# Kernel tuning notes

Measured on AMD Instinct MI355X. Metric: run time of the kernel, lower is better.

Reference implementation:

```python
import jax, jax.numpy as jnp
import numpy as np

B, C, H, W = 8, 256, 64, 64
GROUPS = 32
EPS = 1e-6


def setup_inputs() -> dict:
    key = jax.random.key(0)
    ks = jax.random.split(key, 8)
    s = 0.02
    return {
        "x": jax.random.normal(ks[0], (B, C, H, W), dtype=jnp.float32),
        "gn_scale": jnp.ones((C,), jnp.float32),
        "gn_bias": jnp.zeros((C,), jnp.float32),
        "wq": jax.random.normal(ks[1], (C, C), jnp.float32) * s,
        "bq": jnp.zeros((C,), jnp.float32),
        "wk": jax.random.normal(ks[2], (C, C), jnp.float32) * s,
        "bk": jnp.zeros((C,), jnp.float32),
        "wv": jax.random.normal(ks[3], (C, C), jnp.float32) * s,
        "bv": jnp.zeros((C,), jnp.float32),
        "wproj": jax.random.normal(ks[4], (C, C), jnp.float32) * s,
        "bproj": jnp.zeros((C,), jnp.float32),
    }


def _group_norm(x, scale, bias):
    b, c, h, w = x.shape
    xg = x.reshape(b, GROUPS, c // GROUPS, h, w)
    mean = xg.mean(axis=(2, 3, 4), keepdims=True)
    var = xg.var(axis=(2, 3, 4), keepdims=True)
    xn = ((xg - mean) * jax.lax.rsqrt(var + EPS)).reshape(b, c, h, w)
    return xn * scale[None, :, None, None] + bias[None, :, None, None]


def _conv1x1(x, w, b):
    # 1x1 conv == channel-mixing matmul: w is [out_ch, in_ch]
    return jnp.einsum("oc,bchw->bohw", w, x) + b[None, :, None, None]


def reference(x, gn_scale, gn_bias, wq, bq, wk, bk, wv, bv, wproj, bproj):
    b, c, h, w = x.shape
    hn = _group_norm(x, gn_scale, gn_bias)
    q = _conv1x1(hn, wq, bq).reshape(b, c, h * w)  # [b,c,n]
    k = _conv1x1(hn, wk, bk).reshape(b, c, h * w)
    v = _conv1x1(hn, wv, bv).reshape(b, c, h * w)
    # scores[b,n,m] = <q[:, :, n], k[:, :, m]> * c^-0.5  (softmax over keys m)
    scale = jnp.asarray(c, x.dtype) ** -0.5
    attn = jax.nn.softmax(jnp.einsum("bcn,bcm->bnm", q, k) * scale, axis=2)
    # h_[b,c,n] = sum_m v[b,c,m] * attn[b,n,m]
    h_ = jnp.einsum("bcm,bnm->bcn", v, attn).reshape(b, c, h, w)
    h_ = _conv1x1(h_, wproj, bproj)
    return x + h_
```

## Files before the change

### kernel.cpp

```cpp
#include <hip/hip_runtime.h>

#define B_ 8
#define C_ 256
#define N_ 4096
#define G_ 32

typedef __bf16 bf16;
typedef __bf16 bf16x8 __attribute__((ext_vector_type(8)));
typedef float f32x4 __attribute__((ext_vector_type(4)));
typedef long i64;
typedef long i64x2 __attribute__((ext_vector_type(2)));
typedef unsigned int u32;
typedef unsigned char u8;
typedef unsigned short u16;
typedef unsigned long long u64;
typedef long __attribute__((may_alias)) i64a;

__device__ __forceinline__ f32x4 mfma16(bf16x8 a, bf16x8 b, f32x4 c) {
    return __builtin_amdgcn_mfma_f32_16x16x32_bf16(a, b, c, 0, 0, 0);
}
__device__ __forceinline__ f32x4 mfma_fp8(i64 a, i64 b, f32x4 c) {
    return __builtin_amdgcn_mfma_f32_16x16x32_fp8_fp8(a, b, c, 0, 0, 0);
}

typedef __attribute__((address_space(1))) const void* gas_t;
typedef __attribute__((address_space(3))) void* las_t;
__device__ __forceinline__ void gl2lds16(const void* g, void* l) {
    __builtin_amdgcn_global_load_lds((gas_t)g, (las_t)l, 16, 0, 0);
}

__device__ __forceinline__ u32 f32_to_fp8(float x) {
    union { float f; u32 u; } c;
    c.f = x;
    u32 s = (c.u >> 24) & 0x80;
    u32 m = (c.u & 0x7fffffff) + 0x00080000;
    int e = (int)(m >> 23) - 127;
    if (e < -6) return s;
    if (e > 8) return s | 0x7e;
    u32 v = ((u32)(e + 7) << 3) | ((m >> 20) & 7);
    if (v > 0x7e) v = 0x7e;
    return s | v;
}
__device__ __forceinline__ u32 fp8_fast(float x) {
    union { float f; u32 u; } c;
    c.f = x;
    return ((c.u + 0x00080000u) >> 20) - 960u;
}

__global__ __launch_bounds__(256) void gn_stats(const float* __restrict__ x,
                                                float* __restrict__ gstats) {
    int blk = blockIdx.x;
    int b = blk >> 5, g = blk & 31;
    int tid = threadIdx.x;
    int c = g * 8 + (tid >> 5);
    const float* row = x + ((size_t)(b * C_ + c)) * N_;
    float s = 0.f, s2 = 0.f;
    for (int n = (tid & 31) * 4; n < N_; n += 128) {
        float4 v = *(const float4*)(row + n);
        s += v.x + v.y + v.z + v.w;
        s2 += v.x * v.x + v.y * v.y + v.z * v.z + v.w * v.w;
    }
    for (int off = 32; off; off >>= 1) {
        s += __shfl_xor(s, off);
        s2 += __shfl_xor(s2, off);
    }
    __shared__ float red[8];
    int wid = tid >> 6;
    if ((tid & 63) == 0) { red[wid] = s; red[4 + wid] = s2; }
    __syncthreads();
    if (tid == 0) {
        float S = red[0] + red[1] + red[2] + red[3];
        float S2 = red[4] + red[5] + red[6] + red[7];
        float mean = S * (1.f / 32768.f);
        float var = S2 * (1.f / 32768.f) - mean * mean;
        gstats[blk * 2] = mean;
        gstats[blk * 2 + 1] = rsqrtf(var + 1e-6f);
    }
}

__global__ __launch_bounds__(256) void gn_apply(const float* __restrict__ x,
                                                const float* __restrict__ gsc,
                                                const float* __restrict__ gbi,
                                                const float* __restrict__ gstats,
                                                bf16* __restrict__ hn) {
    __shared__ float tile[32][33];
    int b = blockIdx.z, c0 = blockIdx.y * 32, n0 = blockIdx.x * 32;
    int tx = threadIdx.x & 31, ty = threadIdx.x >> 5;
    for (int i = 0; i < 4; i++) {
        int cl = ty + i * 8;
        int c = c0 + cl;
        int g = c >> 3;
        float mean = gstats[(b * G_ + g) * 2];
        float rstd = gstats[(b * G_ + g) * 2 + 1];
        float sc = gsc[c] * rstd;
        float bs = gbi[c] - mean * sc;
        float v = x[((size_t)(b * C_ + c)) * N_ + n0 + tx];
        tile[cl][tx] = v * sc + bs;
    }
    __syncthreads();
    for (int i = 0; i < 4; i++) {
        int nl = ty + i * 8;
        hn[((size_t)(b * N_ + n0 + nl)) * C_ + c0 + tx] = (bf16)tile[tx][nl];
    }
}

__global__ __launch_bounds__(256) void cvt_w(const float* __restrict__ wq,
                                             const float* __restrict__ wk,
                                             const float* __restrict__ wv,
                                             const float* __restrict__ wp,
                                             bf16* __restrict__ dst) {
    int i = blockIdx.x * 256 + threadIdx.x;
    dst[i] = (bf16)wq[i];
    dst[65536 + i] = (bf16)wk[i];
    dst[131072 + i] = (bf16)wv[i];
    dst[196608 + i] = (bf16)wp[i];
}

__global__ __launch_bounds__(256) void gemm_qkv(const bf16* __restrict__ A,
                                                const bf16* __restrict__ Wq,
                                                const bf16* __restrict__ Wk,
                                                const bf16* __restrict__ Wv,
                                                const float* __restrict__ bq,
                                                const float* __restrict__ bk,
                                                const float* __restrict__ bv,
                                                u8* __restrict__ q8,
                                                u8* __restrict__ k8,
                                                u8* __restrict__ v8) {
    __shared__ __align__(16) bf16 As[64][32];
    __shared__ __align__(16) bf16 Wqs[64][32];
    __shared__ __align__(16) bf16 Wks[64][32];
    __shared__ __align__(16) bf16 Wvs[64][32];
    int m0 = blockIdx.x * 64;
    int n0 = blockIdx.y * 64;
    int tid = threadIdx.x;
    int wv_ = tid >> 6, lane = tid & 63, lr = lane & 15, lq = lane >> 4;
    int wm = (wv_ & 1) * 32, wn = (wv_ >> 1) * 32;
    int sr = tid >> 2, sk = (tid & 3) * 8;
    f32x4 qacc[2][2] = {}, kacc[2][2] = {}, vacc[2][2] = {};
    for (int kk = 0; kk < C_; kk += 32) {
        __syncthreads();
        gl2lds16(&A[(size_t)(m0 + sr) * C_ + kk + sk], &As[sr][sk]);
        gl2lds16(&Wq[(size_t)(n0 + sr) * C_ + kk + sk], &Wqs[sr][sk]);
        gl2lds16(&Wk[(size_t)(n0 + sr) * C_ + kk + sk], &Wks[sr][sk]);
        gl2lds16(&Wv[(size_t)(n0 + sr) * C_ + kk + sk], &Wvs[sr][sk]);
        __syncthreads();
        bf16x8 a0 = *(const bf16x8*)&As[wm + lr][lq * 8];
        bf16x8 a1 = *(const bf16x8*)&As[wm + 16 + lr][lq * 8];
        bf16x8 q0 = *(const bf16x8*)&Wqs[wn + lr][lq * 8];
        bf16x8 q1 = *(const bf16x8*)&Wqs[wn + 16 + lr][lq * 8];
        bf16x8 k0 = *(const bf16x8*)&Wks[wn + lr][lq * 8];
        bf16x8 k1 = *(const bf16x8*)&Wks[wn + 16 + lr][lq * 8];
        bf16x8 v0 = *(const bf16x8*)&Wvs[wn + lr][lq * 8];
        bf16x8 v1 = *(const bf16x8*)&Wvs[wn + 16 + lr][lq * 8];
        qacc[0][0] = mfma16(a0, q0, qacc[0][0]);
        qacc[0][1] = mfma16(a0, q1, qacc[0][1]);
        qacc[1][0] = mfma16(a1, q0, qacc[1][0]);
        qacc[1][1] = mfma16(a1, q1, qacc[1][1]);
        kacc[0][0] = mfma16(a0, k0, kacc[0][0]);
        kacc[0][1] = mfma16(a0, k1, kacc[0][1]);
        kacc[1][0] = mfma16(a1, k0, kacc[1][0]);
        kacc[1][1] = mfma16(a1, k1, kacc[1][1]);
        vacc[0][0] = mfma16(a0, v0, vacc[0][0]);
        vacc[0][1] = mfma16(a0, v1, vacc[0][1]);
        vacc[1][0] = mfma16(a1, v0, vacc[1][0]);
        vacc[1][1] = mfma16(a1, v1, vacc[1][1]);
    }
    for (int i = 0; i < 2; i++)
        for (int j = 0; j < 2; j++) {
            int col = n0 + wn + j * 16 + lr;
            int p = (col & 0xC0) | ((col & 0x18) << 1) | ((col & 0x20) >> 2) | (col & 7);
            float bvq = bq[col], bvk = bk[col], bvv = bv[col];
            for (int r = 0; r < 4; r++) {
                int row = m0 + wm + i * 16 + lq * 4 + r;
                q8[(size_t)row * C_ + p] = (u8)f32_to_fp8(qacc[i][j][r] + bvq);
                k8[(size_t)row * C_ + p] = (u8)f32_to_fp8(kacc[i][j][r] + bvk);
                int bb = row >> 12, n = row & (N_ - 1);
                int n5 = n & 31;
                v8[((size_t)(bb * C_ + col)) * N_ + (n & ~31) +
                   (((n5 & 12) << 1) | ((n5 & 16) >> 2) | (n5 & 3))] =
                    (u8)f32_to_fp8(vacc[i][j][r] + bvv);
            }
        }
}

__global__ __launch_bounds__(128, 2) void attn(const u8* __restrict__ q,
                                               const u8* __restrict__ k,
                                               const u8* __restrict__ vT,
                                               bf16* __restrict__ O0,
                                               bf16* __restrict__ O1,
                                               float* __restrict__ lp) {
    __shared__ __align__(16) u8 smem[32768];
    u8* Ks = smem;
    u8* Vt = smem + 16384;

    int flat = blockIdx.x + (blockIdx.y << 6) + (blockIdx.z << 7);
    int nid = (flat & 7) * 128 + (flat >> 3);
    int q0 = (nid & 63) * 64;
    int h = (nid >> 6) & 1;
    int b = nid >> 7;
    int tid = threadIdx.x;
    int w = tid >> 6, lane = tid & 63, lr = lane & 15, lq = lane >> 4;

    const u8* kglob = k + ((size_t)(b * N_) + h * 2048) * 256;
    const u8* vglob = vT + (size_t)b * C_ * N_ + h * 2048;

    u32 offK[4], offV[4];
#pragma unroll
    for (int j = 0; j < 4; j++) {
        int p = ((w * 4 + j) << 6) + lane;
        int rK = p >> 4, cK = (p & 15) ^ (rK & 15);
        offK[j] = rK * 256 + cK * 16;
        int rV = p >> 1, cV = (p & 1) ^ ((rV >> 2) & 1);
        offV[j] = rV * N_ + cV * 16;
    }

    i64x2 qf[2][4];
#pragma unroll
    for (int t = 0; t < 2; t++) {
        const u8* qrow = q + ((size_t)(b * N_ + q0 + w * 32 + t * 16 + lr)) * 256;
#pragma unroll
        for (int tq = 0; tq < 4; tq++)
            qf[t][tq] = *(const i64x2*)&qrow[tq * 64 + lq * 16];
    }

    f32x4 oacc[2][16] = {};
    float li[2] = {};

#pragma unroll
    for (int j = 0; j < 4; j++) {
        gl2lds16(kglob + offK[j], Ks + ((w * 4 + j) << 10));
        gl2lds16(vglob + offV[j], Vt + ((w * 4 + j) << 10));
    }

    for (int mt = 0; mt < 64; mt++) {
        int cur = mt & 1;
        __syncthreads();

        if (mt < 63) {
            const u8* kit = kglob + (size_t)(mt + 1) * 32 * 256;
            const u8* vit = vglob + (mt + 1) * 32;
#pragma unroll
            for (int j = 0; j < 4; j++) {
                gl2lds16(kit + offK[j], Ks + (cur ^ 1) * 8192 + ((w * 4 + j) << 10));
                gl2lds16(vit + offV[j], Vt + (cur ^ 1) * 8192 + ((w * 4 + j) << 10));
            }
        }

        const u8* Kb = Ks + cur * 8192;
        const u8* Vb = Vt + cur * 8192;

        f32x4 st[2][2] = {};
#pragma unroll
        for (int kt = 0; kt < 2; kt++) {
            int r = kt * 16 + lr;
#pragma unroll
            for (int tq = 0; tq < 4; tq++) {
                i64x2 kf = *(const i64x2*)&Kb[r * 256 + (((tq * 4 + lq) ^ (r & 15)) << 4)];
                st[0][kt] = mfma_fp8(kf.x, qf[0][tq].x, st[0][kt]);
                st[0][kt] = mfma_fp8(kf.y, qf[0][tq].y, st[0][kt]);
                st[1][kt] = mfma_fp8(kf.x, qf[1][tq].x, st[1][kt]);
                st[1][kt] = mfma_fp8(kf.y, qf[1][tq].y, st[1][kt]);
            }
        }

        i64 pf[2];
#pragma unroll
        for (int qt = 0; qt < 2; qt++) {
            float e[2][4];
#pragma unroll
            for (int kt = 0; kt < 2; kt++)
#pragma unroll
                for (int r = 0; r < 4; r++)
                    e[kt][r] = __expf(st[qt][kt][r] * 0.0625f);
            li[qt] += ((e[0][0] + e[0][1]) + (e[0][2] + e[0][3])) +
                      ((e[1][0] + e[1][1]) + (e[1][2] + e[1][3]));
            u32 lo = (fp8_fast(e[0][0]) & 0xff) | ((fp8_fast(e[0][1]) & 0xff) << 8) |
                     ((fp8_fast(e[0][2]) & 0xff) << 16) | (fp8_fast(e[0][3]) << 24);
            u32 hi = (fp8_fast(e[1][0]) & 0xff) | ((fp8_fast(e[1][1]) & 0xff) << 8) |
                     ((fp8_fast(e[1][2]) & 0xff) << 16) | (fp8_fast(e[1][3]) << 24);
            pf[qt] = (i64)(((u64)hi << 32) | lo);
        }

#pragma unroll
        for (int ct = 0; ct < 16; ct++) {
            int row = ct * 16 + lr;
            i64 vf = *(const i64a*)&Vb[row * 32 + (((lq >> 1) ^ ((row >> 2) & 1)) << 4) +
                                       ((lq & 1) << 3)];
            oacc[0][ct] = mfma_fp8(pf[0], vf, oacc[0][ct]);
            oacc[1][ct] = mfma_fp8(pf[1], vf, oacc[1][ct]);
        }
    }

    float lsum[2];
#pragma unroll
    for (int qt = 0; qt < 2; qt++) {
        float s = li[qt];
        s += __shfl_xor(s, 16);
        s += __shfl_xor(s, 32);
        lsum[qt] = s;
    }

    bf16* Op = h ? O1 : O0;
#pragma unroll
    for (int t = 0; t < 2; t++)
#pragma unroll
        for (int ct = 0; ct < 16; ct++)
#pragma unroll
            for (int r = 0; r < 4; r++)
                Op[((size_t)(b * N_ + q0 + w * 32 + t * 16 + lq * 4 + r)) * C_ + ct * 16 + lr] =
                    (bf16)oacc[t][ct][r];
    if (lq == 0) {
        float* lrow = lp + ((size_t)(h * B_ + b)) * N_ + q0 + w * 32;
#pragma unroll
        for (int qt = 0; qt < 2; qt++) lrow[qt * 16 + lr] = lsum[qt];
    }
}

__global__ __launch_bounds__(256) void proj_res(const bf16* __restrict__ W,
                                                const bf16* __restrict__ O0,
                                                const bf16* __restrict__ O1,
                                                const float* __restrict__ lp,
                                                const float* __restrict__ bias,
                                                const float* __restrict__ x,
                                                float* __restrict__ out) {
    __shared__ __align__(16) bf16 Ws[64][32];
    __shared__ __align__(16) bf16 As[64][32];
    int m0 = blockIdx.x * 64;
    int n0 = blockIdx.y * 64;
    int tid = threadIdx.x;
    int wv_ = tid >> 6, lane = tid & 63, lr = lane & 15, lq = lane >> 4;
    int wm = (wv_ & 1) * 32, wn = (wv_ >> 1) * 32;
    int sr = tid >> 2, sk = (tid & 3) * 8;
    int T = n0 + sr, bb = T >> 12, nn = T & (N_ - 1);
    float inv = 1.f / (lp[(size_t)bb * N_ + nn] + lp[(size_t)(B_ + bb) * N_ + nn]);
    f32x4 acc[2][2] = {};
    for (int kk = 0; kk < C_; kk += 32) {
        __syncthreads();
        gl2lds16(&W[(size_t)(m0 + sr) * C_ + kk + sk], &Ws[sr][sk]);
        bf16x8 o0 = *(const bf16x8*)&O0[(size_t)T * C_ + kk + sk];
        bf16x8 o1 = *(const bf16x8*)&O1[(size_t)T * C_ + kk + sk];
        bf16x8 cm;
#pragma unroll
        for (int e = 0; e < 8; e++) cm[e] = (bf16)(((float)o0[e] + (float)o1[e]) * inv);
        *(bf16x8*)&As[sr][sk] = cm;
        __syncthreads();
        bf16x8 a0 = *(const bf16x8*)&Ws[wm + lr][lq * 8];
        bf16x8 a1 = *(const bf16x8*)&Ws[wm + 16 + lr][lq * 8];
        bf16x8 b0 = *(const bf16x8*)&As[wn + lr][lq * 8];
        bf16x8 b1 = *(const bf16x8*)&As[wn + 16 + lr][lq * 8];
        acc[0][0] = mfma16(a0, b0, acc[0][0]);
        acc[0][1] = mfma16(a0, b1, acc[0][1]);
        acc[1][0] = mfma16(a1, b0, acc[1][0]);
        acc[1][1] = mfma16(a1, b1, acc[1][1]);
    }
    for (int i = 0; i < 2; i++)
        for (int j = 0; j < 2; j++) {
            int Tt = n0 + wn + j * 16 + lr;
            int b = Tt >> 12, n = Tt & (N_ - 1);
            for (int r = 0; r < 4; r++) {
                int o = m0 + wm + i * 16 + lq * 4 + r;
                size_t idx = ((size_t)(b * C_ + o)) * N_ + n;
                out[idx] = x[idx] + acc[i][j][r] + bias[o];
            }
        }
}

extern "C" void kernel_launch(void* const* d_in, const int* in_sizes, int n_in,
                              void* d_out, int out_size, void* d_ws, size_t ws_size,
                              hipStream_t stream) {
    const float* x = (const float*)d_in[0];
    const float* gsc = (const float*)d_in[1];
    const float* gbi = (const float*)d_in[2];
    const float* wq = (const float*)d_in[3];
    const float* bq = (const float*)d_in[4];
    const float* wk = (const float*)d_in[5];
    const float* bk = (const float*)d_in[6];
    const float* wv = (const float*)d_in[7];
    const float* bv = (const float*)d_in[8];
    const float* wp = (const float*)d_in[9];
    const float* bp = (const float*)d_in[10];
    float* out = (float*)d_out;

    const size_t SZ = (size_t)B_ * N_ * C_;
    char* ws = (char*)d_ws;
    float* gstats = (float*)ws;
    bf16* wb = (bf16*)(ws + 4096);
    char* base = ws + 4096 + 524288;
    bf16* hn = (bf16*)base;
    u8* q8 = (u8*)(base + SZ * 2);
    u8* k8 = (u8*)(base + SZ * 3);
    u8* v8 = (u8*)(base + SZ * 4);
    bf16* O0 = (bf16*)base;
    bf16* O1 = (bf16*)(base + SZ * 5);
    float* lpart = (float*)(base + SZ * 7);

    cvt_w<<<256, 256, 0, stream>>>(wq, wk, wv, wp, wb);
    gn_stats<<<B_ * G_, 256, 0, stream>>>(x, gstats);
    gn_apply<<<dim3(N_ / 32, C_ / 32, B_), 256, 0, stream>>>(x, gsc, gbi, gstats, hn);
    gemm_qkv<<<dim3(B_ * N_ / 64, C_ / 64), 256, 0, stream>>>(
        hn, wb, wb + 65536, wb + 131072, bq, bk, bv, q8, k8, v8);
    attn<<<dim3(N_ / 64, 2, B_), 128, 0, stream>>>(q8, k8, v8, O0, O1, lpart);
    proj_res<<<dim3(C_ / 64, B_ * N_ / 64), 256, 0, stream>>>(
        wb + 196608, O0, O1, lpart, bp, x, out);
}
```

Before: 306.6 us.

## Software-pipeline QK^T and PV across tiles with triple-buffered V and tiled V layout

The QKV projection now writes V in a tile-blocked layout (32-key tiles of 8 KB with the channel-major interleave), so each attention tile is loaded with contiguous 16-byte copies instead of strided rows. The attention loop is restructured into a two-stage software pipeline: QK^T and softmax of the next key tile are computed while PV for the previous tile runs. V is triple-buffered in LDS, K is double-buffered, and s_setprio raises wave priority around the compute. LDS addressing is precomputed into registers. This raises LDS usage to 40 KB per block and adds register pressure, which could affect occupancy at 2 blocks per CU.

```diff
diff --git a/kernel.cpp b/kernel.cpp
--- a/kernel.cpp
+++ b/kernel.cpp
@@ -175,10 +175,10 @@
                 q8[(size_t)row * C_ + p] = (u8)f32_to_fp8(qacc[i][j][r] + bvq);
                 k8[(size_t)row * C_ + p] = (u8)f32_to_fp8(kacc[i][j][r] + bvk);
                 int bb = row >> 12, n = row & (N_ - 1);
-                int n5 = n & 31;
-                v8[((size_t)(bb * C_ + col)) * N_ + (n & ~31) +
-                   (((n5 & 12) << 1) | ((n5 & 16) >> 2) | (n5 & 3))] =
-                    (u8)f32_to_fp8(vacc[i][j][r] + bvv);
+                int k5 = n & 31;
+                int m = ((k5 & 12) << 1) | ((k5 & 16) >> 2) | (k5 & 3);
+                v8[((size_t)(bb * 128 + (n >> 5))) * 8192 + ((m >> 3) << 11) +
+                   (col << 3) + (m & 7)] = (u8)f32_to_fp8(vacc[i][j][r] + bvv);
             }
         }
 }
@@ -189,7 +189,7 @@
                                                bf16* __restrict__ O0,
                                                bf16* __restrict__ O1,
                                                float* __restrict__ lp) {
-    __shared__ __align__(16) u8 smem[32768];
+    __shared__ __align__(16) u8 smem[40960];
     u8* Ks = smem;
     u8* Vt = smem + 16384;
 
@@ -202,7 +202,7 @@
     int w = tid >> 6, lane = tid & 63, lr = lane & 15, lq = lane >> 4;
 
     const u8* kglob = k + ((size_t)(b * N_) + h * 2048) * 256;
-    const u8* vglob = vT + (size_t)b * C_ * N_ + h * 2048;
+    const u8* vglob = vT + ((size_t)(b * 128) + h * 64) * 8192;
 
     u32 offK[4], offV[4];
 #pragma unroll
@@ -210,9 +210,16 @@
         int p = ((w * 4 + j) << 6) + lane;
         int rK = p >> 4, cK = (p & 15) ^ (rK & 15);
         offK[j] = rK * 256 + cK * 16;
-        int rV = p >> 1, cV = (p & 1) ^ ((rV >> 2) & 1);
-        offV[j] = rV * N_ + cV * 16;
-    }
+        offV[j] = (u32)p << 4;
+    }
+
+    u32 kq[8];
+#pragma unroll
+    for (int kt = 0; kt < 2; kt++)
+#pragma unroll
+        for (int tq = 0; tq < 4; tq++)
+            kq[kt * 4 + tq] = (u32)((kt * 16 + lr) * 256 + (((tq * 4 + lq) ^ lr) << 4));
+    u32 vbase = (u32)(lq * 2048 + lr * 8);
 
     i64x2 qf[2][4];
 #pragma unroll
@@ -225,45 +232,29 @@
 
     f32x4 oacc[2][16] = {};
     float li[2] = {};
-
-#pragma unroll
-    for (int j = 0; j < 4; j++) {
-        gl2lds16(kglob + offK[j], Ks + ((w * 4 + j) << 10));
-        gl2lds16(vglob + offV[j], Vt + ((w * 4 + j) << 10));
-    }
-
-    for (int mt = 0; mt < 64; mt++) {
-        int cur = mt & 1;
-        __syncthreads();
-
-        if (mt < 63) {
-            const u8* kit = kglob + (size_t)(mt + 1) * 32 * 256;
-            const u8* vit = vglob + (mt + 1) * 32;
-#pragma unroll
-            for (int j = 0; j < 4; j++) {
-                gl2lds16(kit + offK[j], Ks + (cur ^ 1) * 8192 + ((w * 4 + j) << 10));
-                gl2lds16(vit + offV[j], Vt + (cur ^ 1) * 8192 + ((w * 4 + j) << 10));
-            }
+    i64 pfA[2], pfB[2];
+
+    auto STAGE = [&](int t, u32 kdst, u32 vdst) {
+        const u8* kg = kglob + (size_t)t * 8192;
+        const u8* vg = vglob + (size_t)t * 8192;
+#pragma unroll
+        for (int j = 0; j < 4; j++) {
+            gl2lds16(kg + offK[j], Ks + kdst + ((w * 4 + j) << 10));
+            gl2lds16(vg + offV[j], Vt + vdst + ((w * 4 + j) << 10));
         }
-
-        const u8* Kb = Ks + cur * 8192;
-        const u8* Vb = Vt + cur * 8192;
-
+    };
+    auto QKT_SM = [&](u32 krd, i64 (&pf)[2]) {
         f32x4 st[2][2] = {};
 #pragma unroll
-        for (int kt = 0; kt < 2; kt++) {
-            int r = kt * 16 + lr;
+        for (int kt = 0; kt < 2; kt++)
 #pragma unroll
             for (int tq = 0; tq < 4; tq++) {
-                i64x2 kf = *(const i64x2*)&Kb[r * 256 + (((tq * 4 + lq) ^ (r & 15)) << 4)];
+                i64x2 kf = *(const i64x2*)&Ks[krd + kq[kt * 4 + tq]];
                 st[0][kt] = mfma_fp8(kf.x, qf[0][tq].x, st[0][kt]);
                 st[0][kt] = mfma_fp8(kf.y, qf[0][tq].y, st[0][kt]);
                 st[1][kt] = mfma_fp8(kf.x, qf[1][tq].x, st[1][kt]);
                 st[1][kt] = mfma_fp8(kf.y, qf[1][tq].y, st[1][kt]);
             }
-        }
-
-        i64 pf[2];
 #pragma unroll
         for (int qt = 0; qt < 2; qt++) {
             float e[2][4];
@@ -280,16 +271,45 @@
                      ((fp8_fast(e[1][2]) & 0xff) << 16) | (fp8_fast(e[1][3]) << 24);
             pf[qt] = (i64)(((u64)hi << 32) | lo);
         }
-
+    };
+    auto PV = [&](u32 vrd, i64 (&pf)[2]) {
 #pragma unroll
         for (int ct = 0; ct < 16; ct++) {
-            int row = ct * 16 + lr;
-            i64 vf = *(const i64a*)&Vb[row * 32 + (((lq >> 1) ^ ((row >> 2) & 1)) << 4) +
-                                       ((lq & 1) << 3)];
+            i64 vf = *(const i64a*)&Vt[vrd + vbase + ct * 128];
             oacc[0][ct] = mfma_fp8(pf[0], vf, oacc[0][ct]);
             oacc[1][ct] = mfma_fp8(pf[1], vf, oacc[1][ct]);
         }
-    }
+    };
+
+    STAGE(0, 0, 0);
+    STAGE(1, 8192, 8192);
+    __syncthreads();
+    QKT_SM(0, pfA);
+
+    u32 vr0 = 0, vr1 = 8192, vr2 = 16384;
+    for (int mt = 0; mt < 62; mt += 2) {
+        __syncthreads();
+        STAGE(mt + 2, 0, vr2);
+        __builtin_amdgcn_s_setprio(1);
+        QKT_SM(8192, pfB);
+        PV(vr0, pfA);
+        __builtin_amdgcn_s_setprio(0);
+        { u32 t = vr0; vr0 = vr1; vr1 = vr2; vr2 = t; }
+        __syncthreads();
+        STAGE(mt + 3, 8192, vr2);
+        __builtin_amdgcn_s_setprio(1);
+        QKT_SM(0, pfA);
+        PV(vr0, pfB);
+        __builtin_amdgcn_s_setprio(0);
+        { u32 t = vr0; vr0 = vr1; vr1 = vr2; vr2 = t; }
+    }
+    __syncthreads();
+    __builtin_amdgcn_s_setprio(1);
+    QKT_SM(8192, pfB);
+    PV(vr0, pfA);
+    { u32 t = vr0; vr0 = vr1; vr1 = vr2; vr2 = t; }
+    PV(vr0, pfB);
+    __builtin_amdgcn_s_setprio(0);
 
     float lsum[2];
 #pragma unroll
```

Result: faster. 293.6 us (-4.2%).

## Switch attention to 32x32x64 scaled FP8 MFMA with new K/V layout and triple-buffering

Applied to the files above, without the earlier changes.

Replaces the 16x16x32 FP8 MFMA attention loop with the gfx950 scaled 32x32x64 f8f6f4 MFMA using unit scales, processing 64 keys per iteration. The QKV kernel writes V in a new per-tile blocked and swizzled layout so that a whole 64-key V tile can be loaded contiguously. K staging moves to a triple-buffered ring with explicit vmcnt waits, raw barriers and setprio around the MFMA region. The aim is higher matrix throughput per instruction and fewer LDS reads per FLOP, at the cost of more LDS (40 KB), a single V buffer that needs an extra barrier, and tricky wait-count correctness.

```diff
diff --git a/kernel.cpp b/kernel.cpp
--- a/kernel.cpp
+++ b/kernel.cpp
@@ -8,19 +8,23 @@
 typedef __bf16 bf16;
 typedef __bf16 bf16x8 __attribute__((ext_vector_type(8)));
 typedef float f32x4 __attribute__((ext_vector_type(4)));
+typedef float f32x16 __attribute__((ext_vector_type(16)));
 typedef long i64;
 typedef long i64x2 __attribute__((ext_vector_type(2)));
+typedef long i64x2a __attribute__((ext_vector_type(2), may_alias));
+typedef int i32x8 __attribute__((ext_vector_type(8)));
+typedef int i32x8a __attribute__((ext_vector_type(8), may_alias));
 typedef unsigned int u32;
 typedef unsigned char u8;
 typedef unsigned short u16;
 typedef unsigned long long u64;
-typedef long __attribute__((may_alias)) i64a;
 
 __device__ __forceinline__ f32x4 mfma16(bf16x8 a, bf16x8 b, f32x4 c) {
     return __builtin_amdgcn_mfma_f32_16x16x32_bf16(a, b, c, 0, 0, 0);
 }
-__device__ __forceinline__ f32x4 mfma_fp8(i64 a, i64 b, f32x4 c) {
-    return __builtin_amdgcn_mfma_f32_16x16x32_fp8_fp8(a, b, c, 0, 0, 0);
+__device__ __forceinline__ f32x16 mfma_mx(i32x8 a, i32x8 b, f32x16 c) {
+    return __builtin_amdgcn_mfma_scale_f32_32x32x64_f8f6f4(
+        a, b, c, 0 , 0 , 0, 0x7F7F7F7F, 0, 0x7F7F7F7F);
 }
 
 typedef __attribute__((address_space(1))) const void* gas_t;
@@ -168,17 +172,18 @@
     for (int i = 0; i < 2; i++)
         for (int j = 0; j < 2; j++) {
             int col = n0 + wn + j * 16 + lr;
-            int p = (col & 0xC0) | ((col & 0x18) << 1) | ((col & 0x20) >> 2) | (col & 7);
             float bvq = bq[col], bvk = bk[col], bvv = bv[col];
             for (int r = 0; r < 4; r++) {
                 int row = m0 + wm + i * 16 + lq * 4 + r;
-                q8[(size_t)row * C_ + p] = (u8)f32_to_fp8(qacc[i][j][r] + bvq);
-                k8[(size_t)row * C_ + p] = (u8)f32_to_fp8(kacc[i][j][r] + bvk);
+                q8[(size_t)row * C_ + col] = (u8)f32_to_fp8(qacc[i][j][r] + bvq);
+                k8[(size_t)row * C_ + col] = (u8)f32_to_fp8(kacc[i][j][r] + bvk);
                 int bb = row >> 12, n = row & (N_ - 1);
-                int n5 = n & 31;
-                v8[((size_t)(bb * C_ + col)) * N_ + (n & ~31) +
-                   (((n5 & 12) << 1) | ((n5 & 16) >> 2) | (n5 & 3))] =
-                    (u8)f32_to_fp8(vacc[i][j][r] + bvv);
+                int h = (n >> 11) & 1, mtl = (n >> 6) & 31, k6 = n & 63;
+                int hbv = (k6 >> 2) & 1;
+                int jv = ((k6 >> 5) << 4) | (((k6 >> 3) & 3) << 2) | (k6 & 3);
+                jv ^= ((col ^ hbv) & 1) << 4;
+                v8[((size_t)(((bb * 2 + h) * 32 + mtl) * 2 + hbv)) * 8192 +
+                   col * 32 + jv] = (u8)f32_to_fp8(vacc[i][j][r] + bvv);
             }
         }
 }
@@ -189,9 +194,7 @@
                                                bf16* __restrict__ O0,
                                                bf16* __restrict__ O1,
                                                float* __restrict__ lp) {
-    __shared__ __align__(16) u8 smem[32768];
-    u8* Ks = smem;
-    u8* Vt = smem + 16384;
+    __shared__ __align__(16) u8 smem[40960];
 
     int flat = blockIdx.x + (blockIdx.y << 6) + (blockIdx.z << 7);
     int nid = (flat & 7) * 128 + (flat >> 3);
@@ -199,121 +202,123 @@
     int h = (nid >> 6) & 1;
     int b = nid >> 7;
     int tid = threadIdx.x;
-    int w = tid >> 6, lane = tid & 63, lr = lane & 15, lq = lane >> 4;
+    int w = tid >> 6, lane = tid & 63, lc = lane & 31, hb = lane >> 5;
 
     const u8* kglob = k + ((size_t)(b * N_) + h * 2048) * 256;
-    const u8* vglob = vT + (size_t)b * C_ * N_ + h * 2048;
-
-    u32 offK[4], offV[4];
+    const u8* vglob = vT + ((size_t)(b * 2 + h)) * 32 * 16384;
+
+    u32 offK[4];
 #pragma unroll
     for (int j = 0; j < 4; j++) {
-        int p = ((w * 4 + j) << 6) + lane;
-        int rK = p >> 4, cK = (p & 15) ^ (rK & 15);
-        offK[j] = rK * 256 + cK * 16;
-        int rV = p >> 1, cV = (p & 1) ^ ((rV >> 2) & 1);
-        offV[j] = rV * N_ + cV * 16;
-    }
-
-    i64x2 qf[2][4];
-#pragma unroll
-    for (int t = 0; t < 2; t++) {
-        const u8* qrow = q + ((size_t)(b * N_ + q0 + w * 32 + t * 16 + lr)) * 256;
-#pragma unroll
-        for (int tq = 0; tq < 4; tq++)
-            qf[t][tq] = *(const i64x2*)&qrow[tq * 64 + lq * 16];
-    }
-
-    f32x4 oacc[2][16] = {};
-    float li[2] = {};
-
-#pragma unroll
-    for (int j = 0; j < 4; j++) {
-        gl2lds16(kglob + offK[j], Ks + ((w * 4 + j) << 10));
-        gl2lds16(vglob + offV[j], Vt + ((w * 4 + j) << 10));
-    }
-
-    for (int mt = 0; mt < 64; mt++) {
-        int cur = mt & 1;
-        __syncthreads();
-
-        if (mt < 63) {
-            const u8* kit = kglob + (size_t)(mt + 1) * 32 * 256;
-            const u8* vit = vglob + (mt + 1) * 32;
-#pragma unroll
-            for (int j = 0; j < 4; j++) {
-                gl2lds16(kit + offK[j], Ks + (cur ^ 1) * 8192 + ((w * 4 + j) << 10));
-                gl2lds16(vit + offV[j], Vt + (cur ^ 1) * 8192 + ((w * 4 + j) << 10));
-            }
-        }
-
-        const u8* Kb = Ks + cur * 8192;
-        const u8* Vb = Vt + cur * 8192;
-
-        f32x4 st[2][2] = {};
-#pragma unroll
-        for (int kt = 0; kt < 2; kt++) {
-            int r = kt * 16 + lr;
-#pragma unroll
-            for (int tq = 0; tq < 4; tq++) {
-                i64x2 kf = *(const i64x2*)&Kb[r * 256 + (((tq * 4 + lq) ^ (r & 15)) << 4)];
-                st[0][kt] = mfma_fp8(kf.x, qf[0][tq].x, st[0][kt]);
-                st[0][kt] = mfma_fp8(kf.y, qf[0][tq].y, st[0][kt]);
-                st[1][kt] = mfma_fp8(kf.x, qf[1][tq].x, st[1][kt]);
-                st[1][kt] = mfma_fp8(kf.y, qf[1][tq].y, st[1][kt]);
-            }
-        }
-
-        i64 pf[2];
-#pragma unroll
-        for (int qt = 0; qt < 2; qt++) {
-            float e[2][4];
-#pragma unroll
-            for (int kt = 0; kt < 2; kt++)
-#pragma unroll
-                for (int r = 0; r < 4; r++)
-                    e[kt][r] = __expf(st[qt][kt][r] * 0.0625f);
-            li[qt] += ((e[0][0] + e[0][1]) + (e[0][2] + e[0][3])) +
-                      ((e[1][0] + e[1][1]) + (e[1][2] + e[1][3]));
-            u32 lo = (fp8_fast(e[0][0]) & 0xff) | ((fp8_fast(e[0][1]) & 0xff) << 8) |
-                     ((fp8_fast(e[0][2]) & 0xff) << 16) | (fp8_fast(e[0][3]) << 24);
-            u32 hi = (fp8_fast(e[1][0]) & 0xff) | ((fp8_fast(e[1][1]) & 0xff) << 8) |
-                     ((fp8_fast(e[1][2]) & 0xff) << 16) | (fp8_fast(e[1][3]) << 24);
-            pf[qt] = (i64)(((u64)hi << 32) | lo);
-        }
-
-#pragma unroll
-        for (int ct = 0; ct < 16; ct++) {
-            int row = ct * 16 + lr;
-            i64 vf = *(const i64a*)&Vb[row * 32 + (((lq >> 1) ^ ((row >> 2) & 1)) << 4) +
-                                       ((lq & 1) << 3)];
-            oacc[0][ct] = mfma_fp8(pf[0], vf, oacc[0][ct]);
-            oacc[1][ct] = mfma_fp8(pf[1], vf, oacc[1][ct]);
-        }
-    }
-
-    float lsum[2];
-#pragma unroll
-    for (int qt = 0; qt < 2; qt++) {
-        float s = li[qt];
-        s += __shfl_xor(s, 16);
-        s += __shfl_xor(s, 32);
-        lsum[qt] = s;
-    }
+        int p = j * 128 + tid;
+        offK[j] = (u32)((p >> 4) * 256 + (((p & 15) ^ ((p >> 4) & 15)) << 4));
+    }
+
+    const u8* qrow = q + ((size_t)(b * N_ + q0 + w * 32 + lc)) * 256 + hb * 32;
+    i32x8 qf[4];
+#pragma unroll
+    for (int kh = 0; kh < 4; kh++) qf[kh] = *(const i32x8a*)&qrow[kh * 64];
+
+    f32x16 oacc[8] = {};
+    float li = 0.f;
+    u32 swz = (u32)(lc & 15);
+    u32 vsw0 = (u32)(((lc ^ hb) & 1) << 4);
+
+    auto STAGE_K = [&](int sidx, int buf) {
+        const u8* kg = kglob + (size_t)sidx * 8192;
+        u8* dst = smem + buf * 8192;
+#pragma unroll
+        for (int j = 0; j < 4; j++)
+            gl2lds16(kg + offK[j], dst + (j * 128 + tid) * 16);
+    };
+    auto STAGE_V = [&](int t) {
+        const u8* vg = vglob + (size_t)t * 16384;
+#pragma unroll
+        for (int j = 0; j < 8; j++)
+            gl2lds16(vg + (j * 128 + tid) * 16, smem + 24576 + (j * 128 + tid) * 16);
+    };
+
+    STAGE_K(0, 0);
+    STAGE_K(1, 1);
+    STAGE_V(0);
+
+    for (int mt = 0; mt < 32; mt++) {
+        int bufa = (2 * mt) % 3, bufb = (2 * mt + 1) % 3, bufc = (2 * mt + 2) % 3;
+        if (mt < 31) {
+            STAGE_K(2 * mt + 2, bufc);
+            asm volatile("s_waitcnt vmcnt(4)" ::: "memory");
+        } else {
+            asm volatile("s_waitcnt vmcnt(0)" ::: "memory");
+        }
+        __builtin_amdgcn_s_barrier();
+
+        const u8* Ka = smem + bufa * 8192;
+        const u8* Kb = smem + bufb * 8192;
+        __builtin_amdgcn_s_setprio(1);
+
+        f32x16 st0 = {}, st1 = {};
+#pragma unroll
+        for (int kh = 0; kh < 4; kh++) {
+            u32 g0 = (u32)(kh * 4 + hb * 2);
+            union { i64x2 h2[2]; i32x8 v; } kf0, kf1;
+            kf0.h2[0] = *(const i64x2a*)&Ka[lc * 256 + ((g0 ^ swz) << 4)];
+            kf0.h2[1] = *(const i64x2a*)&Ka[lc * 256 + (((g0 + 1) ^ swz) << 4)];
+            st0 = mfma_mx(kf0.v, qf[kh], st0);
+            kf1.h2[0] = *(const i64x2a*)&Kb[lc * 256 + ((g0 ^ swz) << 4)];
+            kf1.h2[1] = *(const i64x2a*)&Kb[lc * 256 + (((g0 + 1) ^ swz) << 4)];
+            st1 = mfma_mx(kf1.v, qf[kh], st1);
+        }
+
+        i32x8 pf;
+#pragma unroll
+        for (int t4 = 0; t4 < 4; t4++) {
+            float a0 = __expf(st0[t4 * 4 + 0] * 0.0625f);
+            float a1 = __expf(st0[t4 * 4 + 1] * 0.0625f);
+            float a2 = __expf(st0[t4 * 4 + 2] * 0.0625f);
+            float a3 = __expf(st0[t4 * 4 + 3] * 0.0625f);
+            float b0 = __expf(st1[t4 * 4 + 0] * 0.0625f);
+            float b1 = __expf(st1[t4 * 4 + 1] * 0.0625f);
+            float b2 = __expf(st1[t4 * 4 + 2] * 0.0625f);
+            float b3 = __expf(st1[t4 * 4 + 3] * 0.0625f);
+            li += ((a0 + a1) + (a2 + a3)) + ((b0 + b1) + (b2 + b3));
+            pf[t4] = (int)((fp8_fast(a0) & 0xff) | ((fp8_fast(a1) & 0xff) << 8) |
+                           ((fp8_fast(a2) & 0xff) << 16) | (fp8_fast(a3) << 24));
+            pf[4 + t4] = (int)((fp8_fast(b0) & 0xff) | ((fp8_fast(b1) & 0xff) << 8) |
+                               ((fp8_fast(b2) & 0xff) << 16) | (fp8_fast(b3) << 24));
+        }
+
+        const u8* Vb = smem + 24576;
+#pragma unroll
+        for (int ct = 0; ct < 8; ct++) {
+            u32 base = (u32)(hb * 8192 + (ct * 32 + lc) * 32);
+            union { i64x2 h2[2]; i32x8 v; } vf;
+            vf.h2[0] = *(const i64x2a*)&Vb[base + vsw0];
+            vf.h2[1] = *(const i64x2a*)&Vb[base + (vsw0 ^ 16)];
+            oacc[ct] = mfma_mx(pf, vf.v, oacc[ct]);
+        }
+        __builtin_amdgcn_s_setprio(0);
+
+        if (mt < 31) {
+            asm volatile("s_waitcnt lgkmcnt(0)" ::: "memory");
+            __builtin_amdgcn_s_barrier();
+            STAGE_K(2 * mt + 3, bufa);
+            STAGE_V(mt + 1);
+        }
+    }
+
+    float lsum = li + __shfl_xor(li, 32);
 
     bf16* Op = h ? O1 : O0;
 #pragma unroll
-    for (int t = 0; t < 2; t++)
-#pragma unroll
-        for (int ct = 0; ct < 16; ct++)
-#pragma unroll
-            for (int r = 0; r < 4; r++)
-                Op[((size_t)(b * N_ + q0 + w * 32 + t * 16 + lq * 4 + r)) * C_ + ct * 16 + lr] =
-                    (bf16)oacc[t][ct][r];
-    if (lq == 0) {
-        float* lrow = lp + ((size_t)(h * B_ + b)) * N_ + q0 + w * 32;
-#pragma unroll
-        for (int qt = 0; qt < 2; qt++) lrow[qt * 16 + lr] = lsum[qt];
-    }
+    for (int ct = 0; ct < 8; ct++)
+#pragma unroll
+        for (int r = 0; r < 16; r++) {
+            int qq = (r & 3) + hb * 4 + (r >> 2) * 8;
+            Op[((size_t)(b * N_ + q0 + w * 32 + qq)) * C_ + ct * 32 + lc] =
+                (bf16)oacc[ct][r];
+        }
+    if (hb == 0)
+        lp[((size_t)(h * B_ + b)) * N_ + q0 + w * 32 + lc] = lsum;
 }
 
 __global__ __launch_bounds__(256) void proj_res(const bf16* __restrict__ W,
```

After: 278.1 us. 1.1x faster.
